# Optimization experiments

Measured on AMD Instinct MI355X. Metric: run time of the kernel, lower is better.

Reference implementation:

```python
import jax, jax.numpy as jnp
import numpy as np

HEADS = 16
DIM_HEAD = 64
SCALE = DIM_HEAD ** -0.5
MASK_NEG = 1000000.0


def setup_inputs() -> dict:
    key = jax.random.key(0)
    ks = jax.random.split(key, 6)
    B, N, M, D = 2, 2048, 2048, 1024
    inner = HEADS * DIM_HEAD  # 1024
    x = jax.random.normal(ks[0], (B, N, D), dtype=jnp.float32)
    context = jax.random.normal(ks[1], (B, M, D), dtype=jnp.float32)
    mask = jax.random.randint(ks[2], (B, N), 0, 2, dtype=jnp.int32)
    Wq = jax.random.normal(ks[3], (D, inner), dtype=jnp.float32) * (D ** -0.5)
    Wkv = jax.random.normal(ks[4], (D, 2 * inner), dtype=jnp.float32) * (D ** -0.5)
    Wout = jax.random.normal(ks[5], (inner, D), dtype=jnp.float32) * (inner ** -0.5)
    bout = jnp.zeros((D,), dtype=jnp.float32)
    return {"x": x, "context": context, "mask": mask,
            "Wq": Wq, "Wkv": Wkv, "Wout": Wout, "bout": bout}


def _split_heads(t):
    # [b, n, (h d)] -> [b, h, n, d]
    b, n, _ = t.shape
    return t.reshape(b, n, HEADS, DIM_HEAD).transpose(0, 2, 1, 3)


def reference(x, context, mask, Wq, Wkv, Wout, bout):
    kv = context @ Wkv                      # [b, m, 2*inner]
    k, v = jnp.split(kv, 2, axis=-1)
    q = x @ Wq                              # [b, n, inner]
    q, k, v = _split_heads(q), _split_heads(k), _split_heads(v)
    dots = jnp.einsum('bhnd,bhmd->bhnm', q, k) * SCALE
    # mask is [b, n]: additive penalty per query row (faithful to source)
    dots = dots - (1.0 - mask.astype(jnp.float32))[:, None, :, None] * MASK_NEG
    attn = jax.nn.softmax(dots, axis=-1)
    out = jnp.einsum('bhnm,bhmd->bhnd', attn, v)  # [b, h, n, d]
    b, h, n, d = out.shape
    out = out.transpose(0, 2, 1, 3).reshape(b, n, h * d)
    return out @ Wout + bout
```

## Files before the change

### kernel.cpp

```cpp
#include <hip/hip_runtime.h>
#include <hip/hip_bf16.h>
#include <math.h>

#define BATCH   2
#define NQ      2048
#define NKV     2048
#define DMODEL  1024
#define HEADS   16
#define INNER   1024
#define KVCOLS  2048

typedef short bf16x8 __attribute__((ext_vector_type(8)));
typedef float f32x4  __attribute__((ext_vector_type(4)));

__device__ __forceinline__ short f2bf(float x) {
    __hip_bfloat16 h = __float2bfloat16(x);
    return *reinterpret_cast<short*>(&h);
}
__device__ __forceinline__ float bf2f(short h) {
    unsigned int u = ((unsigned int)(unsigned short)h) << 16;
    float f;
    __builtin_memcpy(&f, &u, 4);
    return f;
}
__device__ __forceinline__ void gl_lds16(const void* g, void* l) {
    __builtin_amdgcn_global_load_lds(
        (const __attribute__((address_space(1))) unsigned int*)g,
        (__attribute__((address_space(3))) unsigned int*)l, 16, 0, 0);
}
__device__ __forceinline__ int sw(int row, int chunk) {
    return row * 64 + ((chunk ^ (row & 7)) << 3);
}

__device__ __forceinline__ void split_chunk(const float* __restrict__ in,
                                            short* __restrict__ hi,
                                            short* __restrict__ lo, int id)
{
    const int i = (id * 256 + (int)threadIdx.x) * 4;
    float4 v = *(const float4*)(in + i);
    short4 h, l;
    h.x = f2bf(v.x); l.x = f2bf(v.x - bf2f(h.x));
    h.y = f2bf(v.y); l.y = f2bf(v.y - bf2f(h.y));
    h.z = f2bf(v.z); l.z = f2bf(v.z - bf2f(h.z));
    h.w = f2bf(v.w); l.w = f2bf(v.w - bf2f(h.w));
    *(short4*)(hi + i) = h;
    *(short4*)(lo + i) = l;
}

__device__ __forceinline__ void tile_transpose_split(
    const float* __restrict__ W, short* __restrict__ Wth, short* __restrict__ Wtl,
    int Kd, int Nd, int bx, int by, int split)
{
    __shared__ float t[32][33];
    const int lx = threadIdx.x & 31, ly = threadIdx.x >> 5;
    #pragma unroll
    for (int j = 0; j < 4; ++j)
        t[ly + j * 8][lx] = W[(size_t)(by * 32 + ly + j * 8) * Nd + bx * 32 + lx];
    __syncthreads();
    #pragma unroll
    for (int j = 0; j < 4; ++j) {
        const float v = t[lx][ly + j * 8];
        const short h = f2bf(v);
        const size_t idx = (size_t)(bx * 32 + ly + j * 8) * Kd + by * 32 + lx;
        Wth[idx] = h;
        if (split) Wtl[idx] = f2bf(v - bf2f(h));
    }
}

__global__ __launch_bounds__(256)
void prep_all(const float* __restrict__ x, const float* __restrict__ ctx,
              const float* __restrict__ Wq, const float* __restrict__ Wkv,
              const float* __restrict__ Wout,
              short* __restrict__ xh, short* __restrict__ xl,
              short* __restrict__ ch, short* __restrict__ cl,
              short* __restrict__ WqTh, short* __restrict__ WqTl,
              short* __restrict__ WkvTh, short* __restrict__ WkvTl,
              short* __restrict__ WoutT)
{
    const int id = blockIdx.x;
    if (id < 4096) {
        split_chunk(x, xh, xl, id);
    } else if (id < 8192) {
        split_chunk(ctx, ch, cl, id - 4096);
    } else {
        const int r = id - 8192;
        if (r < 1024)
            tile_transpose_split(Wq, WqTh, WqTl, 1024, 1024, r & 31, r >> 5, 1);
        else if (r < 3072)
            tile_transpose_split(Wkv, WkvTh, WkvTl, 1024, 2048, (r - 1024) & 63, (r - 1024) >> 6, 1);
        else
            tile_transpose_split(Wout, WoutT, nullptr, 1024, 1024, (r - 3072) & 31, (r - 3072) >> 5, 0);
    }
}

__global__ __launch_bounds__(256)
void qkv_gemm(const short* __restrict__ xh, const short* __restrict__ xl,
              const short* __restrict__ ch, const short* __restrict__ cl,
              const short* __restrict__ WqTh, const short* __restrict__ WqTl,
              const short* __restrict__ WkvTh, const short* __restrict__ WkvTl,
              short* __restrict__ qhp, short* __restrict__ qlp,
              short* __restrict__ khp, short* __restrict__ klp,
              short* __restrict__ vp)
{
    __shared__ short Ash[128 * 32];
    __shared__ short Asl[128 * 32];
    __shared__ short Bsh[128 * 32];
    __shared__ short Bsl[128 * 32];

    const int tid = threadIdx.x;
    const int z = blockIdx.z;
    const int m0 = blockIdx.y * 128, n0 = blockIdx.x * 128;
    const int w = tid >> 6, ln = tid & 63;
    const int wm = (w & 1) * 64, wn = (w >> 1) * 64;
    const int lr = ln & 15, lq = ln >> 4;
    const int terms = (z == 2) ? 1 : 3;

    const short* Ah  = (z == 0) ? xh : ch;
    const short* Al  = (z == 0) ? xl : cl;
    const short* Bth = (z == 0) ? WqTh : (z == 1 ? WkvTh : WkvTh + (size_t)1024 * 1024);
    const short* Btl = (z == 0) ? WqTl : WkvTl;

    f32x4 acc[4][4];
    #pragma unroll
    for (int mt = 0; mt < 4; ++mt)
        #pragma unroll
        for (int nt = 0; nt < 4; ++nt)
            #pragma unroll
            for (int r = 0; r < 4; ++r) acc[mt][nt][r] = 0.0f;

    for (int k0 = 0; k0 < 1024; k0 += 32) {
        __syncthreads();
        #pragma unroll
        for (int it = 0; it < 2; ++it) {
            const int f = it * 256 + tid;
            const int row = f >> 2, c = f & 3;
            const int cg = c ^ ((row >> 1) & 3);
            const size_t ao = (size_t)(m0 + row) * 1024 + k0 + cg * 8;
            const size_t bo = (size_t)(n0 + row) * 1024 + k0 + cg * 8;
            gl_lds16(Ah  + ao, Ash + f * 8);
            gl_lds16(Bth + bo, Bsh + f * 8);
            if (terms == 3) {
                gl_lds16(Al  + ao, Asl + f * 8);
                gl_lds16(Btl + bo, Bsl + f * 8);
            }
        }
        __syncthreads();

        bf16x8 ah[4], bh[4];
        #pragma unroll
        for (int t = 0; t < 4; ++t) {
            const int ar = wm + t * 16 + lr;
            const int br = wn + t * 16 + lr;
            ah[t] = *(const bf16x8*)(Ash + ar * 32 + ((lq ^ ((ar >> 1) & 3)) << 3));
            bh[t] = *(const bf16x8*)(Bsh + br * 32 + ((lq ^ ((br >> 1) & 3)) << 3));
        }
        #pragma unroll
        for (int mt = 0; mt < 4; ++mt)
            #pragma unroll
            for (int nt = 0; nt < 4; ++nt)
                acc[mt][nt] = __builtin_amdgcn_mfma_f32_16x16x32_bf16(
                    ah[mt], bh[nt], acc[mt][nt], 0, 0, 0);

        if (terms == 3) {
            bf16x8 al[4], bl[4];
            #pragma unroll
            for (int t = 0; t < 4; ++t) {
                const int ar = wm + t * 16 + lr;
                const int br = wn + t * 16 + lr;
                al[t] = *(const bf16x8*)(Asl + ar * 32 + ((lq ^ ((ar >> 1) & 3)) << 3));
                bl[t] = *(const bf16x8*)(Bsl + br * 32 + ((lq ^ ((br >> 1) & 3)) << 3));
            }
            #pragma unroll
            for (int mt = 0; mt < 4; ++mt)
                #pragma unroll
                for (int nt = 0; nt < 4; ++nt) {
                    acc[mt][nt] = __builtin_amdgcn_mfma_f32_16x16x32_bf16(
                        ah[mt], bl[nt], acc[mt][nt], 0, 0, 0);
                    acc[mt][nt] = __builtin_amdgcn_mfma_f32_16x16x32_bf16(
                        al[mt], bh[nt], acc[mt][nt], 0, 0, 0);
                }
        }
    }

    const float scale = (z == 0) ? 2.0f : 1.0f;
    short* Chi = (z == 0) ? qhp : (z == 1 ? khp : vp);
    short* Clo = (z == 0) ? qlp : klp;
    #pragma unroll
    for (int mt = 0; mt < 4; ++mt)
        #pragma unroll
        for (int nt = 0; nt < 4; ++nt)
            #pragma unroll
            for (int r = 0; r < 4; ++r) {
                const int row = m0 + wm + mt * 16 + lq * 4 + r;
                const int col = n0 + wn + nt * 16 + lr;
                const float v = acc[mt][nt][r] * scale;
                const short hh = f2bf(v);
                Chi[(size_t)row * 1024 + col] = hh;
                if (z != 2)
                    Clo[(size_t)row * 1024 + col] = f2bf(v - bf2f(hh));
            }
}

__global__ __launch_bounds__(256)
void gemm_out(const short* __restrict__ A, const short* __restrict__ Bt,
              float* __restrict__ C, const float* __restrict__ bias)
{
    __shared__ short As[128 * 64];
    __shared__ short Bs[64 * 64];
    const int tid = threadIdx.x;
    const int m0 = blockIdx.y * 128, n0 = blockIdx.x * 64;
    const int w = tid >> 6, ln = tid & 63;
    const int wm = (w & 1) * 64, wn = (w >> 1) * 32;
    const int lr = ln & 15, lq = ln >> 4;

    f32x4 acc[4][2];
    #pragma unroll
    for (int mt = 0; mt < 4; ++mt)
        #pragma unroll
        for (int nt = 0; nt < 2; ++nt)
            #pragma unroll
            for (int r = 0; r < 4; ++r) acc[mt][nt][r] = 0.0f;

    for (int k0 = 0; k0 < 1024; k0 += 64) {
        __syncthreads();
        #pragma unroll
        for (int it = 0; it < 4; ++it) {
            const int f = it * 256 + tid;
            const int row = f >> 3, c8 = f & 7;
            const int cg = c8 ^ (row & 7);
            gl_lds16(A + (size_t)(m0 + row) * 1024 + k0 + cg * 8, As + f * 8);
        }
        #pragma unroll
        for (int it = 0; it < 2; ++it) {
            const int f = it * 256 + tid;
            const int row = f >> 3, c8 = f & 7;
            const int cg = c8 ^ (row & 7);
            gl_lds16(Bt + (size_t)(n0 + row) * 1024 + k0 + cg * 8, Bs + f * 8);
        }
        __syncthreads();
        #pragma unroll
        for (int ks = 0; ks < 2; ++ks) {
            bf16x8 af[4], bfr[2];
            #pragma unroll
            for (int t = 0; t < 4; ++t) {
                const int ar = wm + t * 16 + lr;
                af[t] = *(const bf16x8*)(As + ar * 64 + (((ks * 4 + lq) ^ (ar & 7)) << 3));
            }
            #pragma unroll
            for (int t = 0; t < 2; ++t) {
                const int br = wn + t * 16 + lr;
                bfr[t] = *(const bf16x8*)(Bs + br * 64 + (((ks * 4 + lq) ^ (br & 7)) << 3));
            }
            #pragma unroll
            for (int mt = 0; mt < 4; ++mt)
                #pragma unroll
                for (int nt = 0; nt < 2; ++nt)
                    acc[mt][nt] = __builtin_amdgcn_mfma_f32_16x16x32_bf16(
                        af[mt], bfr[nt], acc[mt][nt], 0, 0, 0);
        }
    }
    #pragma unroll
    for (int mt = 0; mt < 4; ++mt)
        #pragma unroll
        for (int nt = 0; nt < 2; ++nt)
            #pragma unroll
            for (int r = 0; r < 4; ++r) {
                const int row = m0 + wm + mt * 16 + lq * 4 + r;
                const int col = n0 + wn + nt * 16 + lr;
                C[(size_t)row * 1024 + col] = acc[mt][nt][r] + bias[col];
            }
}

__device__ __forceinline__ void vwrite(int* __restrict__ vt32, int dg4, int slot,
                                       int2 a, int2 b)
{
    const short* as = (const short*)&a;
    const short* bs = (const short*)&b;
    #pragma unroll
    for (int j = 0; j < 4; ++j)
        vt32[(dg4 + j) * 32 + (((slot >> 2) ^ ((dg4 + j) & 7)) << 2) + (slot & 3)] =
            (int)((unsigned short)as[j] | ((unsigned int)(unsigned short)bs[j] << 16));
}

__global__ __launch_bounds__(512, 4)
void flash_v13(const short* __restrict__ qh, const short* __restrict__ ql,
               const short* __restrict__ kh, const short* __restrict__ kl,
               const short* __restrict__ vp, const int* __restrict__ mask,
               short* __restrict__ aob)
{
    const int qt = blockIdx.x, h = blockIdx.y, b = blockIdx.z;
    const int tid = threadIdx.x;
    const int w = tid >> 6, ln = tid & 63;
    const int lr = ln & 15, lq = ln >> 4;
    const int kw = w & 1, wq = w >> 1;

    __shared__ short lds[24576];
    short* Kh = lds;
    short* Kl = lds + 8192;
    short* Vt = lds + 16384;

    const size_t qrow0 = (size_t)(b * NQ + qt * 128);

    bf16x8 aqh[2][2], aql[2][2];
    #pragma unroll
    for (int m = 0; m < 2; ++m)
        #pragma unroll
        for (int ks = 0; ks < 2; ++ks) {
            const size_t qoff = (qrow0 + wq * 32 + m * 16 + lr) * INNER + h * 64 + ks * 32 + lq * 8;
            aqh[m][ks] = *(const bf16x8*)(qh + qoff);
            aql[m][ks] = *(const bf16x8*)(ql + qoff);
        }
    float bmag[2];
    #pragma unroll
    for (int m = 0; m < 2; ++m)
        bmag[m] = mask[b * NQ + qt * 128 + wq * 32 + m * 16 + lr] ? 0.0f : 12582912.0f;

    bf16x8 vone;
    #pragma unroll
    for (int j = 0; j < 8; ++j) vone[j] = (short)0x3F80;

    const int krow = tid >> 3, kc = tid & 7;
    const int kcg = kc ^ (krow & 7);
    const size_t koff0 = ((size_t)(b * NKV + krow)) * INNER + h * 64 + kcg * 8;

    const int idx = tid & 31, dg4 = (tid >> 5) * 4;
    const int tp = idx & 15;
    const int vkey = ((tp >> 2) << 2) + 2 * (tp & 1) + (((tp >> 1) & 1) << 4)
                   + ((idx >> 4) << 5);
    int2 rva, rvb;

    {
        const short* v0 = vp + (size_t)(b * NKV + vkey) * INNER + h * 64 + dg4;
        rva = *(const int2*)(v0);
        rvb = *(const int2*)(v0 + INNER);
        gl_lds16(kh + koff0, Kh + tid * 8);
        gl_lds16(kl + koff0, Kl + tid * 8);
        vwrite((int*)Vt, dg4, idx, rva, rvb);
    }

    f32x4 oacc[2][4];
    #pragma unroll
    for (int m = 0; m < 2; ++m)
        #pragma unroll
        for (int dg = 0; dg < 4; ++dg)
            #pragma unroll
            for (int r = 0; r < 4; ++r) oacc[m][dg][r] = 0.0f;
    f32x4 pacc[2];
    #pragma unroll
    for (int m = 0; m < 2; ++m)
        #pragma unroll
        for (int r = 0; r < 4; ++r) pacc[m][r] = 0.0f;

    const float C16 = 1.44269504f * 0.0625f;

    for (int kt = 0; kt < NKV / 64; ++kt) {
        const int cur = kt & 1;
        __syncthreads();

        if (kt < NKV / 64 - 1) {
            const size_t kadd = (size_t)((kt + 1) * 64) * INNER;
            const short* v0 = vp + (size_t)(b * NKV + (kt + 1) * 64 + vkey) * INNER + h * 64 + dg4;
            rva = *(const int2*)(v0);
            rvb = *(const int2*)(v0 + INNER);
            const int nb = (cur ^ 1) * 4096;
            gl_lds16(kh + koff0 + kadd, Kh + nb + tid * 8);
            gl_lds16(kl + koff0 + kadd, Kl + nb + tid * 8);
        }

        const short* KhC = Kh + cur * 4096;
        const short* KlC = Kl + cur * 4096;
        const short* VtC = Vt + cur * 4096;

        f32x4 sacc[2][2];
        #pragma unroll
        for (int m = 0; m < 2; ++m)
            #pragma unroll
            for (int g2 = 0; g2 < 2; ++g2)
                #pragma unroll
                for (int r = 0; r < 4; ++r) sacc[m][g2][r] = 0.0f;
        __builtin_amdgcn_s_setprio(1);
        #pragma unroll
        for (int ks = 0; ks < 2; ++ks) {
            #pragma unroll
            for (int g2 = 0; g2 < 2; ++g2) {
                const int gg = kw * 2 + g2;
                const bf16x8 bkh = *(const bf16x8*)(KhC + sw(gg * 16 + lr, ks * 4 + lq));
                const bf16x8 bkl = *(const bf16x8*)(KlC + sw(gg * 16 + lr, ks * 4 + lq));
                #pragma unroll
                for (int m = 0; m < 2; ++m) {
                    sacc[m][g2] = __builtin_amdgcn_mfma_f32_16x16x32_bf16(bkh, aqh[m][ks], sacc[m][g2], 0, 0, 0);
                    sacc[m][g2] = __builtin_amdgcn_mfma_f32_16x16x32_bf16(bkl, aqh[m][ks], sacc[m][g2], 0, 0, 0);
                    sacc[m][g2] = __builtin_amdgcn_mfma_f32_16x16x32_bf16(bkh, aql[m][ks], sacc[m][g2], 0, 0, 0);
                }
            }
        }
        __builtin_amdgcn_s_setprio(0);

        bf16x8 ap[2];
        #pragma unroll
        for (int m = 0; m < 2; ++m) {
            bf16x8 a;
            #pragma unroll
            for (int g2 = 0; g2 < 2; ++g2)
                #pragma unroll
                for (int r = 0; r < 4; ++r) {
                    const float sq = (sacc[m][g2][r] + bmag[m]) - bmag[m];
                    const float xx = sq * C16;
                    float pv;
                    asm("v_exp_f32 %0, %1" : "=v"(pv) : "v"(xx));
                    a[g2 * 4 + r] = f2bf(pv);
                }
            ap[m] = a;
        }

        __builtin_amdgcn_s_setprio(1);
        #pragma unroll
        for (int m = 0; m < 2; ++m)
            pacc[m] = __builtin_amdgcn_mfma_f32_16x16x32_bf16(ap[m], vone, pacc[m], 0, 0, 0);
        #pragma unroll
        for (int dg = 0; dg < 4; ++dg) {
            const bf16x8 bv = *(const bf16x8*)(VtC + sw(dg * 16 + lr, kw * 4 + lq));
            oacc[0][dg] = __builtin_amdgcn_mfma_f32_16x16x32_bf16(ap[0], bv, oacc[0][dg], 0, 0, 0);
            oacc[1][dg] = __builtin_amdgcn_mfma_f32_16x16x32_bf16(ap[1], bv, oacc[1][dg], 0, 0, 0);
        }
        __builtin_amdgcn_s_setprio(0);

        if (kt < NKV / 64 - 1) {
            vwrite((int*)(Vt + (cur ^ 1) * 4096), dg4, idx, rva, rvb);
        }
    }

    __syncthreads();
    {
        float* scr = (float*)lds;
        float* slot = scr + (size_t)(wq * 64 + ln) * 40;
        if (kw) {
            #pragma unroll
            for (int m = 0; m < 2; ++m) {
                #pragma unroll
                for (int dg = 0; dg < 4; ++dg)
                    *(f32x4*)(slot + m * 16 + dg * 4) = oacc[m][dg];
                *(f32x4*)(slot + 32 + m * 4) = pacc[m];
            }
        }
        __syncthreads();
        if (!kw) {
            #pragma unroll
            for (int m = 0; m < 2; ++m) {
                #pragma unroll
                for (int dg = 0; dg < 4; ++dg)
                    oacc[m][dg] += *(const f32x4*)(slot + m * 16 + dg * 4);
                pacc[m] += *(const f32x4*)(slot + 32 + m * 4);
            }
            #pragma unroll
            for (int m = 0; m < 2; ++m) {
                float pinv[4];
                #pragma unroll
                for (int r = 0; r < 4; ++r) pinv[r] = 1.0f / pacc[m][r];
                #pragma unroll
                for (int dg = 0; dg < 4; ++dg)
                    #pragma unroll
                    for (int r = 0; r < 4; ++r) {
                        const int row = wq * 32 + m * 16 + lq * 4 + r;
                        aob[(qrow0 + row) * INNER + h * 64 + dg * 16 + lr] =
                            f2bf(oacc[m][dg][r] * pinv[r]);
                    }
            }
        }
    }
}

extern "C" void kernel_launch(void* const* d_in, const int* in_sizes, int n_in,
                              void* d_out, int out_size, void* d_ws, size_t ws_size,
                              hipStream_t stream)
{
    const float* x    = (const float*)d_in[0];
    const float* ctx  = (const float*)d_in[1];
    const int*   mask = (const int*)d_in[2];
    const float* Wq   = (const float*)d_in[3];
    const float* Wkv  = (const float*)d_in[4];
    const float* Wout = (const float*)d_in[5];
    const float* bout = (const float*)d_in[6];
    float* out = (float*)d_out;

    short* base  = (short*)d_ws;
    short* xh    = base;
    short* xl    = base + (size_t)4 * 1024 * 1024;
    short* aob   = xh;
    short* WqTh  = base + (size_t) 8 * 1024 * 1024;
    short* WqTl  = base + (size_t) 9 * 1024 * 1024;
    short* qhp   = base + (size_t)10 * 1024 * 1024;
    short* qlp   = base + (size_t)14 * 1024 * 1024;
    short* WkvTh = base + (size_t)18 * 1024 * 1024;
    short* WkvTl = base + (size_t)20 * 1024 * 1024;
    short* khp   = base + (size_t)22 * 1024 * 1024;
    short* klp   = base + (size_t)26 * 1024 * 1024;
    short* WoutT = base + (size_t)30 * 1024 * 1024;
    short* ch    = base + (size_t)31 * 1024 * 1024;
    short* cl    = base + (size_t)35 * 1024 * 1024;
    short* vp    = base + (size_t)39 * 1024 * 1024;

    const dim3 blk(256);
    prep_all<<<12288, blk, 0, stream>>>(x, ctx, Wq, Wkv, Wout,
                                        xh, xl, ch, cl,
                                        WqTh, WqTl, WkvTh, WkvTl, WoutT);
    qkv_gemm<<<dim3(8, 32, 3), blk, 0, stream>>>(
        xh, xl, ch, cl, WqTh, WqTl, WkvTh, WkvTl,
        qhp, qlp, khp, klp, vp);
    flash_v13<<<dim3(NQ / 128, HEADS, BATCH), dim3(512), 0, stream>>>(
        qhp, qlp, khp, klp, vp, mask, aob);
    gemm_out<<<dim3(1024 / 64, 4096 / 128), blk, 0, stream>>>(
        aob, WoutT, out, bout);
}
```

Before: 254.4 us.

## Double-buffer LDS tiles in QKV and output projection GEMMs

Both projection GEMMs now keep two LDS buffers and prefetch the next K-tile with direct global-to-LDS loads while MFMAs run on the current one. This cuts the two barriers per iteration down to one and hides global load latency behind compute. Source offsets are precomputed once per thread rather than every iteration. Launch bounds now request two blocks per CU, which limits registers per thread, while the doubled shared memory may reduce occupancy or cause spills.

```diff
diff --git a/kernel.cpp b/kernel.cpp
--- a/kernel.cpp
+++ b/kernel.cpp
@@ -93,7 +93,7 @@
     }
 }
 
-__global__ __launch_bounds__(256)
+__global__ __launch_bounds__(256, 2)
 void qkv_gemm(const short* __restrict__ xh, const short* __restrict__ xl,
               const short* __restrict__ ch, const short* __restrict__ cl,
               const short* __restrict__ WqTh, const short* __restrict__ WqTl,
@@ -102,10 +102,10 @@
               short* __restrict__ khp, short* __restrict__ klp,
               short* __restrict__ vp)
 {
-    __shared__ short Ash[128 * 32];
-    __shared__ short Asl[128 * 32];
-    __shared__ short Bsh[128 * 32];
-    __shared__ short Bsl[128 * 32];
+    __shared__ short Ash[2 * 4096];
+    __shared__ short Asl[2 * 4096];
+    __shared__ short Bsh[2 * 4096];
+    __shared__ short Bsl[2 * 4096];
 
     const int tid = threadIdx.x;
     const int z = blockIdx.z;
@@ -120,6 +120,28 @@
     const short* Bth = (z == 0) ? WqTh : (z == 1 ? WkvTh : WkvTh + (size_t)1024 * 1024);
     const short* Btl = (z == 0) ? WqTl : WkvTl;
 
+    int sdst[2]; size_t sao[2], sbo[2];
+    #pragma unroll
+    for (int it = 0; it < 2; ++it) {
+        const int f = it * 256 + tid;
+        const int row = f >> 2, c = f & 3;
+        const int cg = c ^ ((row >> 1) & 3);
+        sdst[it] = f * 8;
+        sao[it] = (size_t)(m0 + row) * 1024 + cg * 8;
+        sbo[it] = (size_t)(n0 + row) * 1024 + cg * 8;
+    }
+    auto STAGE = [&](int k0, int nb) {
+        #pragma unroll
+        for (int it = 0; it < 2; ++it) {
+            gl_lds16(Ah  + sao[it] + k0, Ash + nb + sdst[it]);
+            gl_lds16(Bth + sbo[it] + k0, Bsh + nb + sdst[it]);
+            if (terms == 3) {
+                gl_lds16(Al  + sao[it] + k0, Asl + nb + sdst[it]);
+                gl_lds16(Btl + sbo[it] + k0, Bsl + nb + sdst[it]);
+            }
+        }
+    };
+
     f32x4 acc[4][4];
     #pragma unroll
     for (int mt = 0; mt < 4; ++mt)
@@ -128,31 +150,25 @@
             #pragma unroll
             for (int r = 0; r < 4; ++r) acc[mt][nt][r] = 0.0f;
 
-    for (int k0 = 0; k0 < 1024; k0 += 32) {
+    STAGE(0, 0);
+
+    for (int t = 0; t < 32; ++t) {
+        const int cur = (t & 1) * 4096;
         __syncthreads();
-        #pragma unroll
-        for (int it = 0; it < 2; ++it) {
-            const int f = it * 256 + tid;
-            const int row = f >> 2, c = f & 3;
-            const int cg = c ^ ((row >> 1) & 3);
-            const size_t ao = (size_t)(m0 + row) * 1024 + k0 + cg * 8;
-            const size_t bo = (size_t)(n0 + row) * 1024 + k0 + cg * 8;
-            gl_lds16(Ah  + ao, Ash + f * 8);
-            gl_lds16(Bth + bo, Bsh + f * 8);
-            if (terms == 3) {
-                gl_lds16(Al  + ao, Asl + f * 8);
-                gl_lds16(Btl + bo, Bsl + f * 8);
-            }
-        }
-        __syncthreads();
+        if (t < 31) STAGE((t + 1) * 32, cur ^ 4096);
+
+        const short* AshC = Ash + cur;
+        const short* AslC = Asl + cur;
+        const short* BshC = Bsh + cur;
+        const short* BslC = Bsl + cur;
 
         bf16x8 ah[4], bh[4];
         #pragma unroll
-        for (int t = 0; t < 4; ++t) {
-            const int ar = wm + t * 16 + lr;
-            const int br = wn + t * 16 + lr;
-            ah[t] = *(const bf16x8*)(Ash + ar * 32 + ((lq ^ ((ar >> 1) & 3)) << 3));
-            bh[t] = *(const bf16x8*)(Bsh + br * 32 + ((lq ^ ((br >> 1) & 3)) << 3));
+        for (int tt = 0; tt < 4; ++tt) {
+            const int ar = wm + tt * 16 + lr;
+            const int br = wn + tt * 16 + lr;
+            ah[tt] = *(const bf16x8*)(AshC + ar * 32 + ((lq ^ ((ar >> 1) & 3)) << 3));
+            bh[tt] = *(const bf16x8*)(BshC + br * 32 + ((lq ^ ((br >> 1) & 3)) << 3));
         }
         #pragma unroll
         for (int mt = 0; mt < 4; ++mt)
@@ -164,11 +180,11 @@
         if (terms == 3) {
             bf16x8 al[4], bl[4];
             #pragma unroll
-            for (int t = 0; t < 4; ++t) {
-                const int ar = wm + t * 16 + lr;
-                const int br = wn + t * 16 + lr;
-                al[t] = *(const bf16x8*)(Asl + ar * 32 + ((lq ^ ((ar >> 1) & 3)) << 3));
-                bl[t] = *(const bf16x8*)(Bsl + br * 32 + ((lq ^ ((br >> 1) & 3)) << 3));
+            for (int tt = 0; tt < 4; ++tt) {
+                const int ar = wm + tt * 16 + lr;
+                const int br = wn + tt * 16 + lr;
+                al[tt] = *(const bf16x8*)(AslC + ar * 32 + ((lq ^ ((ar >> 1) & 3)) << 3));
+                bl[tt] = *(const bf16x8*)(BslC + br * 32 + ((lq ^ ((br >> 1) & 3)) << 3));
             }
             #pragma unroll
             for (int mt = 0; mt < 4; ++mt)
@@ -201,18 +217,45 @@
             }
 }
 
-__global__ __launch_bounds__(256)
+__global__ __launch_bounds__(256, 2)
 void gemm_out(const short* __restrict__ A, const short* __restrict__ Bt,
               float* __restrict__ C, const float* __restrict__ bias)
 {
-    __shared__ short As[128 * 64];
-    __shared__ short Bs[64 * 64];
+    __shared__ short As[2 * 8192];
+    __shared__ short Bs[2 * 4096];
     const int tid = threadIdx.x;
     const int m0 = blockIdx.y * 128, n0 = blockIdx.x * 64;
     const int w = tid >> 6, ln = tid & 63;
     const int wm = (w & 1) * 64, wn = (w >> 1) * 32;
     const int lr = ln & 15, lq = ln >> 4;
 
+    int adst[4]; size_t asrc[4];
+    #pragma unroll
+    for (int it = 0; it < 4; ++it) {
+        const int f = it * 256 + tid;
+        const int row = f >> 3, c8 = f & 7;
+        const int cg = c8 ^ (row & 7);
+        adst[it] = f * 8;
+        asrc[it] = (size_t)(m0 + row) * 1024 + cg * 8;
+    }
+    int bdst[2]; size_t bsrc[2];
+    #pragma unroll
+    for (int it = 0; it < 2; ++it) {
+        const int f = it * 256 + tid;
+        const int row = f >> 3, c8 = f & 7;
+        const int cg = c8 ^ (row & 7);
+        bdst[it] = f * 8;
+        bsrc[it] = (size_t)(n0 + row) * 1024 + cg * 8;
+    }
+    auto STAGE = [&](int k0, int ba, int bb) {
+        #pragma unroll
+        for (int it = 0; it < 4; ++it)
+            gl_lds16(A + asrc[it] + k0, As + ba + adst[it]);
+        #pragma unroll
+        for (int it = 0; it < 2; ++it)
+            gl_lds16(Bt + bsrc[it] + k0, Bs + bb + bdst[it]);
+    };
+
     f32x4 acc[4][2];
     #pragma unroll
     for (int mt = 0; mt < 4; ++mt)
@@ -221,35 +264,27 @@
             #pragma unroll
             for (int r = 0; r < 4; ++r) acc[mt][nt][r] = 0.0f;
 
-    for (int k0 = 0; k0 < 1024; k0 += 64) {
+    STAGE(0, 0, 0);
+
+    for (int t = 0; t < 16; ++t) {
+        const int ba = (t & 1) * 8192, bb = (t & 1) * 4096;
         __syncthreads();
-        #pragma unroll
-        for (int it = 0; it < 4; ++it) {
-            const int f = it * 256 + tid;
-            const int row = f >> 3, c8 = f & 7;
-            const int cg = c8 ^ (row & 7);
-            gl_lds16(A + (size_t)(m0 + row) * 1024 + k0 + cg * 8, As + f * 8);
-        }
-        #pragma unroll
-        for (int it = 0; it < 2; ++it) {
-            const int f = it * 256 + tid;
-            const int row = f >> 3, c8 = f & 7;
-            const int cg = c8 ^ (row & 7);
-            gl_lds16(Bt + (size_t)(n0 + row) * 1024 + k0 + cg * 8, Bs + f * 8);
-        }
-        __syncthreads();
+        if (t < 15) STAGE((t + 1) * 64, ba ^ 8192, bb ^ 4096);
+
+        const short* AsC = As + ba;
+        const short* BsC = Bs + bb;
         #pragma unroll
         for (int ks = 0; ks < 2; ++ks) {
             bf16x8 af[4], bfr[2];
             #pragma unroll
-            for (int t = 0; t < 4; ++t) {
-                const int ar = wm + t * 16 + lr;
-                af[t] = *(const bf16x8*)(As + ar * 64 + (((ks * 4 + lq) ^ (ar & 7)) << 3));
-            }
-            #pragma unroll
-            for (int t = 0; t < 2; ++t) {
-                const int br = wn + t * 16 + lr;
-                bfr[t] = *(const bf16x8*)(Bs + br * 64 + (((ks * 4 + lq) ^ (br & 7)) << 3));
+            for (int tt = 0; tt < 4; ++tt) {
+                const int ar = wm + tt * 16 + lr;
+                af[tt] = *(const bf16x8*)(AsC + ar * 64 + (((ks * 4 + lq) ^ (ar & 7)) << 3));
+            }
+            #pragma unroll
+            for (int tt = 0; tt < 2; ++tt) {
+                const int br = wn + tt * 16 + lr;
+                bfr[tt] = *(const bf16x8*)(BsC + br * 64 + (((ks * 4 + lq) ^ (br & 7)) << 3));
             }
             #pragma unroll
             for (int mt = 0; mt < 4; ++mt)
```

Measured after the change: 266.8 us. +4.9%, slower.
